# Kernel tuning notes

Measured on AMD Instinct MI355X. Metric: run time of the kernel, lower is better.

## Reference

```python
import jax, jax.numpy as jnp
import numpy as np

B, C, N, D = 8192, 1000, 2, 512
EPS = 0.1  # epsilon init arg


def setup_inputs() -> dict:
    key = jax.random.key(0)
    kx, kc, kr = jax.random.split(key, 3)
    x = jax.random.normal(kx, (B, D), dtype=jnp.float32)
    centroids = jax.random.uniform(kc, (C, N, D), minval=-1.0, maxval=1.0, dtype=jnp.float32)
    rej_raw = jax.random.uniform(kr, (C * N, D), minval=-1.0, maxval=1.0, dtype=jnp.float32)
    # replicate the __init__ rescaling of the (frozen) rejective centroids
    cmax = jnp.max(jnp.linalg.norm(centroids, axis=-1))
    rej = 2.0 * cmax * rej_raw / (jnp.linalg.norm(rej_raw, axis=-1, keepdims=True) + 1e-16)
    return {"x": x, "centroids": centroids, "rejective_centroids": rej, "return_dists": 1}


def reference(x, centroids, rejective_centroids, return_dists):
    b, d = x.shape
    c, n, _ = centroids.shape
    t = c * n
    # centroid_norm is updated via .data in torch -> detached
    cnorm = jax.lax.stop_gradient(jnp.max(jnp.linalg.norm(centroids, axis=-1)))
    cf = (centroids / (cnorm + 1e-16)).reshape(t, d)  # [T, D] normalized centroids
    # pairwise L2 distances via the expansion identity (no [B,T,D] intermediate)
    x2 = jnp.sum(x * x, axis=-1)          # [B]
    c2 = jnp.sum(cf * cf, axis=-1)        # [T]
    d2 = jnp.maximum(x2[:, None] + c2[None, :] - 2.0 * (x @ cf.T), 0.0)
    dist = jnp.sqrt(d2)                   # [B, T]
    min_dist_class = jnp.min(dist.reshape(b, c, n), axis=2)  # [B, C]
    y = -min_dist_class
    if return_dists:
        idx = jnp.argmin(dist, axis=1)                 # [B]
        closest = cf[idx]                              # [B, D] gathered closest centroid
        r = rejective_centroids                        # [T, D]
        r2 = jnp.sum(r * r, axis=-1)                   # [T]
        xr = x @ r.T                                   # [B, T]
        cr = closest @ r.T                             # [B, T]
        cx = jnp.sum(closest * x, axis=-1)             # [B]
        cl2 = jnp.sum(closest * closest, axis=-1)      # [B]
        # w = closest - r ; b_off = -w . (closest + r)/2 = -0.5(|c|^2 - |r|^2)
        num = jnp.abs(cx[:, None] - xr - 0.5 * (cl2[:, None] - r2[None, :]))
        den = jnp.sqrt(jnp.maximum(cl2[:, None] + r2[None, :] - 2.0 * cr, 0.0)) + 1e-9
        rej_hd = jnp.min(num / den, axis=-1)           # [B]
        return jnp.concatenate([y, rej_hd[:, None]], axis=1)
    min_d = jnp.min(min_dist_class, axis=1)
    removed = jnp.where(min_dist_class == min_d[:, None], jnp.inf, min_dist_class)
    second = jnp.min(removed, axis=1)
    y_bot = -(1.0 - EPS) / (1.0 + EPS) * second
    accept = min_d - EPS * (min_d + second)
    soft = jax.nn.sigmoid(accept)  # ac_temp == 1
    return jnp.concatenate([y, y_bot[:, None], soft[:, None]], axis=1)
```

## Files before the change

kernel.cpp:

```cpp
#include <hip/hip_runtime.h>
#include <math.h>
#include <stdint.h>

#define NB   8192
#define NCLS 1000
#define NT   2000
#define ND   512
#define OUTW 1001

#define OFF_NORM2C 0
#define OFF_R2     2048
#define OFF_X2     4096
#define OFF_SCAL   12288
#define OFF_IDX    12352
#define OFF_CX     20544
#define OFF_CL2    28736

#define NOFF_MIND  36928
#define NOFF_REJP  823360

#define OFF8_MIND  36928
#define OFF8_MINT  102464
#define OFF8_MDOT  168000
#define OFF8_REJP  233536

#define PACKX_B  (8ull<<20)
#define PACKC_B  (24ull<<20)
#define PACKR_B  (28ull<<20)
#define PACKT_B  (32ull<<20)
#define WS_NEED  (48ull<<20)

typedef __attribute__((ext_vector_type(8))) short bf16x8;
typedef __attribute__((ext_vector_type(4))) float f32x4;

__global__ __launch_bounds__(64) void rownorm_kernel(
    const float* __restrict__ cen, const float* __restrict__ rej,
    const float* __restrict__ x, float* __restrict__ ws)
{
    int row = blockIdx.x;
    int lane = threadIdx.x;
    const float* src;
    int dstoff;
    if (row < NT)        { src = cen + (size_t)row * ND;          dstoff = OFF_NORM2C + row; }
    else if (row < 2*NT) { src = rej + (size_t)(row - NT) * ND;   dstoff = OFF_R2 + (row - NT); }
    else                 { src = x   + (size_t)(row - 2*NT) * ND; dstoff = OFF_X2 + (row - 2*NT); }
    float s = 0.f;
#pragma unroll
    for (int k = 0; k < ND / 64; ++k) { float v = src[lane + k * 64]; s += v * v; }
#pragma unroll
    for (int off = 32; off > 0; off >>= 1) s += __shfl_down(s, off);
    if (lane == 0) ws[dstoff] = s;
}

__global__ __launch_bounds__(256) void maxnorm_kernel(float* __restrict__ ws)
{
    __shared__ float sm[256];
    int tid = threadIdx.x;
    float m = 0.f;
    for (int i = tid; i < NT; i += 256) m = fmaxf(m, ws[OFF_NORM2C + i]);
    sm[tid] = m;
    __syncthreads();
    for (int s = 128; s > 0; s >>= 1) {
        if (tid < s) sm[tid] = fmaxf(sm[tid], sm[tid + s]);
        __syncthreads();
    }
    if (tid == 0) {
        float cnorm = sqrtf(sm[0]);
        float inv = 1.f / (cnorm + 1e-16f);
        ws[OFF_SCAL + 0] = cnorm;
        ws[OFF_SCAL + 1] = inv;
        ws[OFF_SCAL + 2] = inv * inv;
    }
}

__device__ __forceinline__ ushort bf16rn(float f){
    uint32_t u = __float_as_uint(f);
    return (ushort)((u + 0x7fffu + ((u >> 16) & 1u)) >> 16);
}

__global__ __launch_bounds__(256) void pack_kernel(const float* __restrict__ src,
    unsigned char* __restrict__ dst, int validRows)
{
    int tid = threadIdx.x;
    int lane = tid & 63;
    int W = blockIdx.x * 4 + (tid >> 6);
    int s  = W >> 4;
    int ks = W & 15;
    int row = s * 16 + (lane & 15);
    int k   = ks * 32 + (lane >> 4) * 8;
    float v[8];
    if (row < validRows) {
        float4 a = *(const float4*)&src[(size_t)row * ND + k];
        float4 b = *(const float4*)&src[(size_t)row * ND + k + 4];
        v[0]=a.x; v[1]=a.y; v[2]=a.z; v[3]=a.w;
        v[4]=b.x; v[5]=b.y; v[6]=b.z; v[7]=b.w;
    } else {
#pragma unroll
        for (int j = 0; j < 8; ++j) v[j] = 0.f;
    }
    union { ushort h[8]; uint4 q; } H, L;
#pragma unroll
    for (int j = 0; j < 8; ++j) {
        ushort hb = bf16rn(v[j]);
        float hf = __uint_as_float(((uint32_t)hb) << 16);
        H.h[j] = hb;
        L.h[j] = bf16rn(v[j] - hf);
    }
    size_t base = ((size_t)(((s >> 3) * 16 + ks) * 16 + (s & 7) * 2)) * 1024;
    *(uint4*)(dst + base + lane * 16)        = H.q;
    *(uint4*)(dst + base + 1024 + lane * 16) = L.q;
}

typedef __attribute__((address_space(3))) unsigned int lds_u32;
typedef const __attribute__((address_space(1))) unsigned int glb_u32;
__device__ __forceinline__ void gload_lds16(const unsigned char* g, unsigned char* l) {
    __builtin_amdgcn_global_load_lds((glb_u32*)g, (lds_u32*)l, 16, 0, 0);
}

template<bool BLO>
__device__ __forceinline__ void stage256(
    const unsigned char* __restrict__ aP2, const unsigned char* __restrict__ bP2,
    int ks, unsigned char* lbuf, int wave, int lane)
{
    if (wave < 4) {
#pragma unroll
        for (int j = 0; j < 8; ++j) {
            int gc = wave * 8 + j;
            gload_lds16(aP2 + (gc >> 4) * 262144 + ks * 16384 + (gc & 15) * 1024 + lane * 16,
                        lbuf + gc * 1024);
        }
    } else {
        if constexpr (BLO) {
#pragma unroll
            for (int j = 0; j < 8; ++j) {
                int gc = (wave - 4) * 8 + j;
                gload_lds16(bP2 + (gc >> 4) * 262144 + ks * 16384 + (gc & 15) * 1024 + lane * 16,
                            lbuf + 32768 + gc * 1024);
            }
        } else {
#pragma unroll
            for (int j = 0; j < 4; ++j) {
                int gc = (wave - 4) * 4 + j;
                gload_lds16(bP2 + (gc >> 3) * 262144 + ks * 16384 + ((gc & 7) * 2) * 1024 + lane * 16,
                            lbuf + 32768 + gc * 1024);
            }
        }
    }
}

#define PASS8(av, bv) do { _Pragma("unroll") \
    for (int qi = 0; qi < 4; ++qi) \
        _Pragma("unroll") \
        for (int ri = 0; ri < 8; ++ri) \
            acc[ri][qi] = __builtin_amdgcn_mfma_f32_16x16x32_bf16( \
                av[ri], bv[qi], acc[ri][qi], 0, 0, 0); \
    } while (0)

template<bool BLO>
__device__ __forceinline__ void compute_step256(
    const unsigned char* __restrict__ cbuf, int lane, int wr, int wc, f32x4 acc[8][4])
{
    const unsigned char* aB = cbuf + wr * 16384 + lane * 16;
    const unsigned char* bB = BLO
        ? cbuf + 32768 + (wc >> 1) * 16384 + ((wc & 1) * 4) * 2048 + lane * 16
        : cbuf + 32768 + (wc >> 1) * 8192  + ((wc & 1) * 4) * 1024 + lane * 16;
    bf16x8 bh[4];
#pragma unroll
    for (int qi = 0; qi < 4; ++qi) bh[qi] = *(const bf16x8*)(bB + qi * (BLO ? 2048 : 1024));
    if constexpr (BLO) {
        bf16x8 bl[4];
#pragma unroll
        for (int qi = 0; qi < 4; ++qi) bl[qi] = *(const bf16x8*)(bB + qi * 2048 + 1024);
        {
            bf16x8 a[8];
#pragma unroll
            for (int ri = 0; ri < 8; ++ri) a[ri] = *(const bf16x8*)(aB + ri * 2048);
            PASS8(a, bh);
            PASS8(a, bl);
        }
        {
            bf16x8 a[8];
#pragma unroll
            for (int ri = 0; ri < 8; ++ri) a[ri] = *(const bf16x8*)(aB + ri * 2048 + 1024);
            PASS8(a, bh);
        }
    } else {
        {
            bf16x8 a[8];
#pragma unroll
            for (int ri = 0; ri < 8; ++ri) a[ri] = *(const bf16x8*)(aB + ri * 2048);
            PASS8(a, bh);
        }
        {
            bf16x8 a[8];
#pragma unroll
            for (int ri = 0; ri < 8; ++ri) a[ri] = *(const bf16x8*)(aB + ri * 2048 + 1024);
            PASS8(a, bh);
        }
    }
}

template<bool BLO>
__device__ __forceinline__ void mfma_core256(
    const unsigned char* __restrict__ aP2, const unsigned char* __restrict__ bP2,
    unsigned char* lds, int lane, int wave, int wr, int wc, f32x4 acc[8][4])
{
    for (int ks = 0; ks < 16; ++ks) {
        stage256<BLO>(aP2, bP2, ks, lds, wave, lane);
        __syncthreads();
        compute_step256<BLO>(lds, lane, wr, wc, acc);
        __syncthreads();
    }
}

__global__ __launch_bounds__(512, 2) void dist_mfma_kernel(
    const unsigned char* __restrict__ xpack, const unsigned char* __restrict__ cpack,
    float* __restrict__ out, float* __restrict__ ws)
{
    __shared__ unsigned char lds[65536];
    int tid = threadIdx.x, lane = tid & 63, wave = tid >> 6;
    int wr = wave >> 2, wc = wave & 3;
    int xb = blockIdx.x, yb = blockIdx.y;
    int b0 = xb * 256, t0base = yb * 256;
    f32x4 acc[8][4];
#pragma unroll
    for (int i = 0; i < 8; ++i)
#pragma unroll
        for (int q = 0; q < 4; ++q) acc[i][q] = (f32x4){0.f, 0.f, 0.f, 0.f};
    mfma_core256<true>(xpack + (size_t)xb * 524288, cpack + (size_t)yb * 524288,
                       lds, lane, wave, wr, wc, acc);

    float inv  = ws[OFF_SCAL + 1];
    float inv2 = ws[OFF_SCAL + 2];
    int rq = lane >> 4, cidx = lane & 15;
    int seg = yb * 4 + wc;
    float c2q[4]; int tq[4];
#pragma unroll
    for (int qi = 0; qi < 4; ++qi) {
        int t = t0base + wc * 64 + qi * 16 + cidx;
        tq[qi] = t;
        c2q[qi] = (t < NT) ? ws[OFF_NORM2C + t] * inv2 : 0.f;
    }
    unsigned long long* keys = (unsigned long long*)(ws + NOFF_MIND);

#pragma unroll
    for (int ri = 0; ri < 8; ++ri) {
#pragma unroll
        for (int reg = 0; reg < 4; ++reg) {
            int row = b0 + wr * 128 + ri * 16 + rq * 4 + reg;
            float x2 = ws[OFF_X2 + row];
            unsigned long long best = ~0ull;
#pragma unroll
            for (int qi = 0; qi < 4; ++qi) {
                float dsc = acc[ri][qi][reg] * inv;
                float dd = sqrtf(fmaxf(x2 + c2q[qi] - 2.f * dsc, 0.f));
                float dn = __shfl_xor(dd, 1);
                int t = tq[qi];
                if ((t < NT) && ((cidx & 1) == 0))
                    out[(size_t)row * OUTW + (t >> 1)] = -fminf(dd, dn);
                if (t < NT) {
                    unsigned long long key =
                        ((unsigned long long)__float_as_uint(dd) << 32) | (unsigned)t;
                    best = best < key ? best : key;
                }
            }
#pragma unroll
            for (int off = 1; off < 16; off <<= 1) {
                unsigned long long o = __shfl_xor(best, off);
                best = best < o ? best : o;
            }
            if (cidx == 0) keys[(size_t)row * 32 + seg] = best;
        }
    }
}

__global__ __launch_bounds__(256) void combine32_kernel(float* __restrict__ ws)
{
    int b = blockIdx.x * 256 + threadIdx.x;
    const unsigned long long* keys = (const unsigned long long*)(ws + NOFF_MIND);
    unsigned long long best = keys[(size_t)b * 32];
#pragma unroll
    for (int s = 1; s < 32; ++s) {
        unsigned long long k = keys[(size_t)b * 32 + s];
        best = best < k ? best : k;
    }
    int bt = (int)(best & 0xffffffffull);
    float dd = __uint_as_float((unsigned)(best >> 32));
    float c2 = ws[OFF_NORM2C + bt] * ws[OFF_SCAL + 2];
    float x2 = ws[OFF_X2 + b];
    ((int*)ws)[OFF_IDX + b] = bt;
    ws[OFF_CX + b] = 0.5f * (x2 + c2 - dd * dd);
    ws[OFF_CL2 + b] = c2;
}

#define LOADA(buf, ks_) do { _Pragma("unroll") \
    for (int i = 0; i < 4; ++i) { \
        buf[i]     = *(const bf16x8*)(aB + (ks_) * 16384 + i * 2048); \
        buf[4 + i] = *(const bf16x8*)(aB + (ks_) * 16384 + i * 2048 + 1024); \
    } } while (0)
#define LOADB2(buf, ks_) do { _Pragma("unroll") \
    for (int i = 0; i < 4; ++i) { \
        buf[i] = *(const bf16x8*)(bB + (ks_) * 16384 + i * 2048); \
    } } while (0)
#define PASS(av, bv, AOFF, BOFF) do { _Pragma("unroll") \
    for (int qi = 0; qi < 4; ++qi) \
        _Pragma("unroll") \
        for (int ri = 0; ri < 4; ++ri) \
            acc[ri][qi] = __builtin_amdgcn_mfma_f32_16x16x32_bf16( \
                av[(AOFF) + ri], bv[(BOFF) + qi], acc[ri][qi], 0, 0, 0); \
    } while (0)
#define COMPUTE2(av, bv) do { PASS(av, bv, 0, 0); PASS(av, bv, 4, 0); } while (0)

__device__ __forceinline__ void mfma_core_db2(
    const unsigned char* __restrict__ aP, const unsigned char* __restrict__ bP,
    int lane, int wr, int wc, f32x4 acc[4][4])
{
    const unsigned char* aB = aP + wr * 8192 + lane * 16;
    const unsigned char* bB = bP + wc * 8192 + lane * 16;
    bf16x8 a0[8], a1[8], b0[4], b1[4];
    LOADA(a0, 0); LOADB2(b0, 0);
    for (int ks = 0; ks < 16; ks += 2) {
        LOADA(a1, ks + 1); LOADB2(b1, ks + 1);
        COMPUTE2(a0, b0);
        if (ks + 2 < 16) { LOADA(a0, ks + 2); LOADB2(b0, ks + 2); }
        COMPUTE2(a1, b1);
    }
}

__global__ __launch_bounds__(256, 2) void table_mfma_kernel(
    const unsigned char* __restrict__ cpack, const unsigned char* __restrict__ rpack,
    float* __restrict__ table, const float* __restrict__ ws)
{
    int tid = threadIdx.x, lane = tid & 63, wave = tid >> 6;
    int wr = wave >> 1, wc = wave & 1;
    int c0 = blockIdx.x * 128, t0base = blockIdx.y * 128;
    f32x4 acc[4][4];
#pragma unroll
    for (int i = 0; i < 4; ++i)
#pragma unroll
        for (int q = 0; q < 4; ++q) acc[i][q] = (f32x4){0.f, 0.f, 0.f, 0.f};
    mfma_core_db2(cpack + (size_t)blockIdx.x * 262144, rpack + (size_t)blockIdx.y * 262144,
                  lane, wr, wc, acc);

    float inv  = ws[OFF_SCAL + 1];
    float inv2 = ws[OFF_SCAL + 2];
    int rq = lane >> 4, cidx = lane & 15;
    float r2q[4]; int tq[4];
#pragma unroll
    for (int qi = 0; qi < 4; ++qi) {
        int t = t0base + wc * 64 + qi * 16 + cidx;
        tq[qi] = t;
        r2q[qi] = (t < NT) ? ws[OFF_R2 + t] : 0.f;
    }
#pragma unroll
    for (int ri = 0; ri < 4; ++ri) {
#pragma unroll
        for (int reg = 0; reg < 4; ++reg) {
            int c = c0 + wr * 64 + ri * 16 + rq * 4 + reg;
            if (c < NT) {
                float cl2c = ws[OFF_NORM2C + c] * inv2;
#pragma unroll
                for (int qi = 0; qi < 4; ++qi) {
                    int t = tq[qi];
                    if (t < NT) {
                        float cfr = acc[ri][qi][reg] * inv;
                        float den = sqrtf(fmaxf(cl2c + r2q[qi] - 2.f * cfr, 0.f)) + 1e-9f;
                        table[(size_t)c * 2048 + t] = 1.f / den;
                    }
                }
            }
        }
    }
}

__global__ __launch_bounds__(512, 2) void xr_mfma_kernel(
    const unsigned char* __restrict__ xpack, const unsigned char* __restrict__ rpack,
    const float* __restrict__ table, float* __restrict__ ws)
{
    __shared__ unsigned char lds[49152];
    int tid = threadIdx.x, lane = tid & 63, wave = tid >> 6;
    int wr = wave >> 2, wc = wave & 3;
    int xb = blockIdx.x, yb = blockIdx.y;
    int b0 = xb * 256, t0base = yb * 256;
    f32x4 acc[8][4];
#pragma unroll
    for (int i = 0; i < 8; ++i)
#pragma unroll
        for (int q = 0; q < 4; ++q) acc[i][q] = (f32x4){0.f, 0.f, 0.f, 0.f};
    mfma_core256<false>(xpack + (size_t)xb * 524288, rpack + (size_t)yb * 524288,
                        lds, lane, wave, wr, wc, acc);

    int rq = lane >> 4, cidx = lane & 15;
    int seg = yb * 4 + wc;
    float r2q[4]; int tq[4];
#pragma unroll
    for (int qi = 0; qi < 4; ++qi) {
        int t = t0base + wc * 64 + qi * 16 + cidx;
        tq[qi] = t;
        r2q[qi] = (t < NT) ? ws[OFF_R2 + t] : 0.f;
    }
#pragma unroll
    for (int ri = 0; ri < 8; ++ri) {
#pragma unroll
        for (int reg = 0; reg < 4; ++reg) {
            int row = b0 + wr * 128 + ri * 16 + rq * 4 + reg;
            int idx = ((const int*)ws)[OFF_IDX + row];
            float cx  = ws[OFF_CX + row];
            float cl2 = ws[OFF_CL2 + row];
            const float* trow = table + (size_t)idx * 2048;
            float mv = INFINITY;
#pragma unroll
            for (int qi = 0; qi < 4; ++qi) {
                int t = tq[qi];
                if (t < NT) {
                    float num = fabsf(cx - acc[ri][qi][reg] - 0.5f * (cl2 - r2q[qi]));
                    mv = fminf(mv, num * trow[t]);
                }
            }
#pragma unroll
            for (int off = 1; off < 16; off <<= 1) mv = fminf(mv, __shfl_xor(mv, off));
            if (cidx == 0) ws[NOFF_REJP + (size_t)row * 32 + seg] = mv;
        }
    }
}

__global__ __launch_bounds__(256) void rejcombine32_kernel(
    const float* __restrict__ ws, float* __restrict__ out)
{
    int b = blockIdx.x * 256 + threadIdx.x;
    float bd = ws[NOFF_REJP + (size_t)b * 32];
#pragma unroll
    for (int s = 1; s < 32; ++s) bd = fminf(bd, ws[NOFF_REJP + (size_t)b * 32 + s]);
    out[(size_t)b * OUTW + NCLS] = bd;
}

#define BK   32
#define LDST 68

__global__ __launch_bounds__(256) void dist_kernel(
    const float* __restrict__ x, const float* __restrict__ cen,
    float* __restrict__ out, float* __restrict__ ws)
{
    __shared__ float Xs[BK][LDST];
    __shared__ float Cs[BK][LDST];
    __shared__ float red_d[64][17];
    __shared__ int   red_t[64][17];
    __shared__ float red_x[64][17];

    int tid = threadIdx.x;
    int tx = tid & 15, ty = tid >> 4;
    int b0 = blockIdx.x * 64;
    int tseg0 = blockIdx.y * 256;
    int tseg1 = min(tseg0 + 256, NT);

    float inv  = ws[OFF_SCAL + 1];
    float inv2 = ws[OFF_SCAL + 2];
    float x2v[4];
#pragma unroll
    for (int i = 0; i < 4; ++i) x2v[i] = ws[OFF_X2 + b0 + ty * 4 + i];

    int lr = tid >> 2;
    int lc = (tid & 3) * 8;

    float mind[4], mdot[4];
    int mint[4];
#pragma unroll
    for (int i = 0; i < 4; ++i) { mind[i] = INFINITY; mint[i] = 0x7fffffff; mdot[i] = 0.f; }

    for (int t0 = tseg0; t0 < tseg1; t0 += 64) {
        float acc[4][4];
#pragma unroll
        for (int i = 0; i < 4; ++i)
#pragma unroll
            for (int jj = 0; jj < 4; ++jj) acc[i][jj] = 0.f;

        for (int k0 = 0; k0 < ND; k0 += BK) {
            {
                const float4 v0 = *(const float4*)&x[(size_t)(b0 + lr) * ND + k0 + lc];
                const float4 v1 = *(const float4*)&x[(size_t)(b0 + lr) * ND + k0 + lc + 4];
                Xs[lc + 0][lr] = v0.x; Xs[lc + 1][lr] = v0.y; Xs[lc + 2][lr] = v0.z; Xs[lc + 3][lr] = v0.w;
                Xs[lc + 4][lr] = v1.x; Xs[lc + 5][lr] = v1.y; Xs[lc + 6][lr] = v1.z; Xs[lc + 7][lr] = v1.w;
            }
            {
                int tr = t0 + lr;
                float4 v0 = make_float4(0.f, 0.f, 0.f, 0.f), v1 = v0;
                if (tr < NT) {
                    v0 = *(const float4*)&cen[(size_t)tr * ND + k0 + lc];
                    v1 = *(const float4*)&cen[(size_t)tr * ND + k0 + lc + 4];
                }
                Cs[lc + 0][lr] = v0.x; Cs[lc + 1][lr] = v0.y; Cs[lc + 2][lr] = v0.z; Cs[lc + 3][lr] = v0.w;
                Cs[lc + 4][lr] = v1.x; Cs[lc + 5][lr] = v1.y; Cs[lc + 6][lr] = v1.z; Cs[lc + 7][lr] = v1.w;
            }
            __syncthreads();
#pragma unroll
            for (int kk = 0; kk < BK; ++kk) {
                float4 av = *(const float4*)&Xs[kk][ty * 4];
                float4 bv = *(const float4*)&Cs[kk][tx * 4];
                float a[4] = {av.x, av.y, av.z, av.w};
                float bb[4] = {bv.x, bv.y, bv.z, bv.w};
#pragma unroll
                for (int i = 0; i < 4; ++i)
#pragma unroll
                    for (int jj = 0; jj < 4; ++jj)
                        acc[i][jj] = fmaf(a[i], bb[jj], acc[i][jj]);
            }
            __syncthreads();
        }

        float distv[4][4];
#pragma unroll
        for (int jj = 0; jj < 4; ++jj) {
            int t = t0 + tx * 4 + jj;
            bool valid = (t < NT);
            float c2 = valid ? ws[OFF_NORM2C + t] * inv2 : 0.f;
#pragma unroll
            for (int i = 0; i < 4; ++i) {
                float dsc = acc[i][jj] * inv;
                float d2 = x2v[i] + c2 - 2.f * dsc;
                float dd = sqrtf(fmaxf(d2, 0.f));
                distv[i][jj] = dd;
                if (valid && (dd < mind[i])) { mind[i] = dd; mint[i] = t; mdot[i] = dsc; }
            }
        }
#pragma unroll
        for (int jp = 0; jp < 2; ++jp) {
            int t = t0 + tx * 4 + jp * 2;
            if (t < NT) {
                int cls = t >> 1;
#pragma unroll
                for (int i = 0; i < 4; ++i) {
                    out[(size_t)(b0 + ty * 4 + i) * OUTW + cls] =
                        -fminf(distv[i][jp * 2], distv[i][jp * 2 + 1]);
                }
            }
        }
    }

#pragma unroll
    for (int i = 0; i < 4; ++i) {
        red_d[ty * 4 + i][tx] = mind[i];
        red_t[ty * 4 + i][tx] = mint[i];
        red_x[ty * 4 + i][tx] = mdot[i];
    }
    __syncthreads();
    if (tid < 64) {
        float bd = red_d[tid][0]; int bt = red_t[tid][0]; float bx = red_x[tid][0];
        for (int q = 1; q < 16; ++q) {
            float d = red_d[tid][q]; int tt = red_t[tid][q];
            if (d < bd || (d == bd && tt < bt)) { bd = d; bt = tt; bx = red_x[tid][q]; }
        }
        int b = b0 + tid;
        int s = blockIdx.y;
        ws[OFF8_MIND + b * 8 + s] = bd;
        ((int*)ws)[OFF8_MINT + b * 8 + s] = bt;
        ws[OFF8_MDOT + b * 8 + s] = bx;
    }
}

__global__ __launch_bounds__(256) void combine_kernel(float* __restrict__ ws)
{
    int b = blockIdx.x * 256 + threadIdx.x;
    float bd = ws[OFF8_MIND + b * 8];
    int   bt = ((int*)ws)[OFF8_MINT + b * 8];
    float bx = ws[OFF8_MDOT + b * 8];
#pragma unroll
    for (int s = 1; s < 8; ++s) {
        float d = ws[OFF8_MIND + b * 8 + s];
        int  tt = ((int*)ws)[OFF8_MINT + b * 8 + s];
        if (d < bd || (d == bd && tt < bt)) { bd = d; bt = tt; bx = ws[OFF8_MDOT + b * 8 + s]; }
    }
    ((int*)ws)[OFF_IDX + b] = bt;
    ws[OFF_CX + b] = bx;
    ws[OFF_CL2 + b] = ws[OFF_NORM2C + bt] * ws[OFF_SCAL + 2];
}

__global__ __launch_bounds__(256) void rej_kernel(
    const float* __restrict__ x, const float* __restrict__ cen,
    const float* __restrict__ rej, float* __restrict__ ws)
{
    __shared__ float Xs[BK][LDST];
    __shared__ float Rs[BK][LDST];
    __shared__ float Ls[BK][LDST];
    __shared__ int idxL[64];
    __shared__ float red_d[64][17];

    int tid = threadIdx.x;
    int tx = tid & 15, ty = tid >> 4;
    int b0 = blockIdx.x * 64;
    int tseg0 = blockIdx.y * 256;
    int tseg1 = min(tseg0 + 256, NT);
    float inv = ws[OFF_SCAL + 1];

    if (tid < 64) idxL[tid] = ((int*)ws)[OFF_IDX + b0 + tid];
    float cxv[4], cl2v[4];
#pragma unroll
    for (int i = 0; i < 4; ++i) {
        cxv[i]  = ws[OFF_CX  + b0 + ty * 4 + i];
        cl2v[i] = ws[OFF_CL2 + b0 + ty * 4 + i];
    }
    __syncthreads();

    int lr = tid >> 2, lc = (tid & 3) * 8;
    int myrow = idxL[lr];

    float minv[4] = {INFINITY, INFINITY, INFINITY, INFINITY};

    for (int t0 = tseg0; t0 < tseg1; t0 += 64) {
        float xr[4][4], cr[4][4];
#pragma unroll
        for (int i = 0; i < 4; ++i)
#pragma unroll
            for (int jj = 0; jj < 4; ++jj) { xr[i][jj] = 0.f; cr[i][jj] = 0.f; }

        for (int k0 = 0; k0 < ND; k0 += BK) {
            {
                const float4 v0 = *(const float4*)&x[(size_t)(b0 + lr) * ND + k0 + lc];
                const float4 v1 = *(const float4*)&x[(size_t)(b0 + lr) * ND + k0 + lc + 4];
                Xs[lc + 0][lr] = v0.x; Xs[lc + 1][lr] = v0.y; Xs[lc + 2][lr] = v0.z; Xs[lc + 3][lr] = v0.w;
                Xs[lc + 4][lr] = v1.x; Xs[lc + 5][lr] = v1.y; Xs[lc + 6][lr] = v1.z; Xs[lc + 7][lr] = v1.w;
            }
            {
                const float4 v0 = *(const float4*)&cen[(size_t)myrow * ND + k0 + lc];
                const float4 v1 = *(const float4*)&cen[(size_t)myrow * ND + k0 + lc + 4];
                Ls[lc + 0][lr] = v0.x * inv; Ls[lc + 1][lr] = v0.y * inv;
                Ls[lc + 2][lr] = v0.z * inv; Ls[lc + 3][lr] = v0.w * inv;
                Ls[lc + 4][lr] = v1.x * inv; Ls[lc + 5][lr] = v1.y * inv;
                Ls[lc + 6][lr] = v1.z * inv; Ls[lc + 7][lr] = v1.w * inv;
            }
            {
                int tr = t0 + lr;
                float4 v0 = make_float4(0.f, 0.f, 0.f, 0.f), v1 = v0;
                if (tr < NT) {
                    v0 = *(const float4*)&rej[(size_t)tr * ND + k0 + lc];
                    v1 = *(const float4*)&rej[(size_t)tr * ND + k0 + lc + 4];
                }
                Rs[lc + 0][lr] = v0.x; Rs[lc + 1][lr] = v0.y; Rs[lc + 2][lr] = v0.z; Rs[lc + 3][lr] = v0.w;
                Rs[lc + 4][lr] = v1.x; Rs[lc + 5][lr] = v1.y; Rs[lc + 6][lr] = v1.z; Rs[lc + 7][lr] = v1.w;
            }
            __syncthreads();
#pragma unroll
            for (int kk = 0; kk < BK; ++kk) {
                float4 av = *(const float4*)&Xs[kk][ty * 4];
                float4 lv = *(const float4*)&Ls[kk][ty * 4];
                float4 rv = *(const float4*)&Rs[kk][tx * 4];
                float a[4] = {av.x, av.y, av.z, av.w};
                float l[4] = {lv.x, lv.y, lv.z, lv.w};
                float r[4] = {rv.x, rv.y, rv.z, rv.w};
#pragma unroll
                for (int i = 0; i < 4; ++i)
#pragma unroll
                    for (int jj = 0; jj < 4; ++jj) {
                        xr[i][jj] = fmaf(a[i], r[jj], xr[i][jj]);
                        cr[i][jj] = fmaf(l[i], r[jj], cr[i][jj]);
                    }
            }
            __syncthreads();
        }

#pragma unroll
        for (int jj = 0; jj < 4; ++jj) {
            int t = t0 + tx * 4 + jj;
            if (t < NT) {
                float r2 = ws[OFF_R2 + t];
#pragma unroll
                for (int i = 0; i < 4; ++i) {
                    float num = fabsf(cxv[i] - xr[i][jj] - 0.5f * (cl2v[i] - r2));
                    float den = sqrtf(fmaxf(cl2v[i] + r2 - 2.f * cr[i][jj], 0.f)) + 1e-9f;
                    minv[i] = fminf(minv[i], num / den);
                }
            }
        }
    }

#pragma unroll
    for (int i = 0; i < 4; ++i) red_d[ty * 4 + i][tx] = minv[i];
    __syncthreads();
    if (tid < 64) {
        float bd = red_d[tid][0];
        for (int q = 1; q < 16; ++q) bd = fminf(bd, red_d[tid][q]);
        ws[OFF8_REJP + (size_t)(b0 + tid) * 8 + blockIdx.y] = bd;
    }
}

__global__ __launch_bounds__(256) void rejcombine_kernel(
    const float* __restrict__ ws, float* __restrict__ out)
{
    int b = blockIdx.x * 256 + threadIdx.x;
    float bd = ws[OFF8_REJP + b * 8];
#pragma unroll
    for (int s = 1; s < 8; ++s) bd = fminf(bd, ws[OFF8_REJP + b * 8 + s]);
    out[(size_t)b * OUTW + NCLS] = bd;
}

extern "C" void kernel_launch(void* const* d_in, const int* in_sizes, int n_in,
                              void* d_out, int out_size, void* d_ws, size_t ws_size,
                              hipStream_t stream)
{
    const float* x   = (const float*)d_in[0];
    const float* cen = (const float*)d_in[1];
    const float* rej = (const float*)d_in[2];
    float* out = (float*)d_out;
    float* ws  = (float*)d_ws;
    unsigned char* wsb = (unsigned char*)d_ws;

    rownorm_kernel<<<2 * NT + NB, 64, 0, stream>>>(cen, rej, x, ws);
    maxnorm_kernel<<<1, 256, 0, stream>>>(ws);

    if (ws_size >= WS_NEED) {
        pack_kernel<<<2048, 256, 0, stream>>>(x,   wsb + PACKX_B, NB);
        pack_kernel<<<512,  256, 0, stream>>>(cen, wsb + PACKC_B, NT);
        pack_kernel<<<512,  256, 0, stream>>>(rej, wsb + PACKR_B, NT);
        dist_mfma_kernel<<<dim3(32, 8), 512, 0, stream>>>(wsb + PACKX_B, wsb + PACKC_B, out, ws);
        combine32_kernel<<<32, 256, 0, stream>>>(ws);
        table_mfma_kernel<<<dim3(16, 16), 256, 0, stream>>>(wsb + PACKC_B, wsb + PACKR_B,
                                                            (float*)(wsb + PACKT_B), ws);
        xr_mfma_kernel<<<dim3(32, 8), 512, 0, stream>>>(wsb + PACKX_B, wsb + PACKR_B,
                                                        (float*)(wsb + PACKT_B), ws);
        rejcombine32_kernel<<<32, 256, 0, stream>>>(ws, out);
    } else {
        dist_kernel<<<dim3(NB / 64, 8), 256, 0, stream>>>(x, cen, out, ws);
        combine_kernel<<<NB / 256, 256, 0, stream>>>(ws);
        rej_kernel<<<dim3(NB / 64, 8), 256, 0, stream>>>(x, cen, rej, ws);
        rejcombine_kernel<<<NB / 256, 256, 0, stream>>>(ws, out);
    }
}
```

Baseline: 186.6 us.

## Double-buffer LDS staging in MFMA GEMM loops with manual waitcnt

Replaces the synchronous stage/compute loop with a double-buffered pipeline that issues global loads for the next K-step into a second LDS buffer while computing the current one. It uses explicit vmcnt waits, sched barriers, raw s_barrier calls, and raises wave priority around MFMA compute. LDS doubles to 128KB and 96KB per block and the launch bounds drop the 2-blocks-per-CU hint, so occupancy falls to one block per CU. The hand-written vmcnt counts depend on how many loads stage256 issues per wave.

Result: no change. 185.5 us (-0.6%).

```diff
diff --git a/kernel.cpp b/kernel.cpp
--- a/kernel.cpp
+++ b/kernel.cpp
@@ -200,24 +200,42 @@
     }
 }
 
+#define SCHED_FENCE __builtin_amdgcn_sched_barrier(0)
+
 template<bool BLO>
-__device__ __forceinline__ void mfma_core256(
+__device__ __forceinline__ void mfma_core256_pipe(
     const unsigned char* __restrict__ aP2, const unsigned char* __restrict__ bP2,
     unsigned char* lds, int lane, int wave, int wr, int wc, f32x4 acc[8][4])
 {
+    constexpr int BUF = BLO ? 65536 : 49152;
+    stage256<BLO>(aP2, bP2, 0, lds, wave, lane);
     for (int ks = 0; ks < 16; ++ks) {
-        stage256<BLO>(aP2, bP2, ks, lds, wave, lane);
-        __syncthreads();
-        compute_step256<BLO>(lds, lane, wr, wc, acc);
-        __syncthreads();
-    }
-}
-
-__global__ __launch_bounds__(512, 2) void dist_mfma_kernel(
+        unsigned char* cbuf = lds + (ks & 1) * BUF;
+        unsigned char* nbuf = lds + ((ks + 1) & 1) * BUF;
+        if (ks < 15) {
+            stage256<BLO>(aP2, bP2, ks + 1, nbuf, wave, lane);
+            SCHED_FENCE;
+            if (BLO || wave < 4) asm volatile("s_waitcnt vmcnt(8)" ::: "memory");
+            else                 asm volatile("s_waitcnt vmcnt(4)" ::: "memory");
+            SCHED_FENCE;
+        } else {
+            SCHED_FENCE;
+            asm volatile("s_waitcnt vmcnt(0)" ::: "memory");
+            SCHED_FENCE;
+        }
+        __builtin_amdgcn_s_barrier();
+        __builtin_amdgcn_s_setprio(1);
+        compute_step256<BLO>(cbuf, lane, wr, wc, acc);
+        __builtin_amdgcn_s_setprio(0);
+        __builtin_amdgcn_s_barrier();
+    }
+}
+
+__global__ __launch_bounds__(512) void dist_mfma_kernel(
     const unsigned char* __restrict__ xpack, const unsigned char* __restrict__ cpack,
     float* __restrict__ out, float* __restrict__ ws)
 {
-    __shared__ unsigned char lds[65536];
+    __shared__ unsigned char lds[2 * 65536];
     int tid = threadIdx.x, lane = tid & 63, wave = tid >> 6;
     int wr = wave >> 2, wc = wave & 3;
     int xb = blockIdx.x, yb = blockIdx.y;
@@ -227,8 +245,8 @@
     for (int i = 0; i < 8; ++i)
 #pragma unroll
         for (int q = 0; q < 4; ++q) acc[i][q] = (f32x4){0.f, 0.f, 0.f, 0.f};
-    mfma_core256<true>(xpack + (size_t)xb * 524288, cpack + (size_t)yb * 524288,
-                       lds, lane, wave, wr, wc, acc);
+    mfma_core256_pipe<true>(xpack + (size_t)xb * 524288, cpack + (size_t)yb * 524288,
+                            lds, lane, wave, wr, wc, acc);
 
     float inv  = ws[OFF_SCAL + 1];
     float inv2 = ws[OFF_SCAL + 2];
@@ -373,11 +391,11 @@
     }
 }
 
-__global__ __launch_bounds__(512, 2) void xr_mfma_kernel(
+__global__ __launch_bounds__(512) void xr_mfma_kernel(
     const unsigned char* __restrict__ xpack, const unsigned char* __restrict__ rpack,
     const float* __restrict__ table, float* __restrict__ ws)
 {
-    __shared__ unsigned char lds[49152];
+    __shared__ unsigned char lds[2 * 49152];
     int tid = threadIdx.x, lane = tid & 63, wave = tid >> 6;
     int wr = wave >> 2, wc = wave & 3;
     int xb = blockIdx.x, yb = blockIdx.y;
@@ -387,8 +405,8 @@
     for (int i = 0; i < 8; ++i)
 #pragma unroll
         for (int q = 0; q < 4; ++q) acc[i][q] = (f32x4){0.f, 0.f, 0.f, 0.f};
-    mfma_core256<false>(xpack + (size_t)xb * 524288, rpack + (size_t)yb * 524288,
-                        lds, lane, wave, wr, wc, acc);
+    mfma_core256_pipe<false>(xpack + (size_t)xb * 524288, rpack + (size_t)yb * 524288,
+                             lds, lane, wave, wr, wc, acc);
 
     int rq = lane >> 4, cidx = lane & 15;
     int seg = yb * 4 + wc;
```
